# Optimization experiments

Measured on AMD Instinct MI355X. Metric: run time of the kernel, lower is better.

Reference implementation:

```python
import jax, jax.numpy as jnp
import numpy as np

N_DRUG = 20000
N_TARGET = 20000
N = N_DRUG + N_TARGET
E = 500000
D = 128
L = 2
NEG_SLOPE = 0.2


def _gat(h, edge_index, W, asrc, adst, edge_bias=None):
    """Single-head GAT layer: h [N,d] -> [N,d]."""
    n = h.shape[0]
    hp = h @ W                                   # [N,d]
    src, dst = edge_index[0], edge_index[1]      # [E]
    logit = (hp @ asrc)[src] + (hp @ adst)[dst]  # [E]
    if edge_bias is not None:
        logit = logit + edge_bias
    e = jax.nn.leaky_relu(logit, NEG_SLOPE)
    # numerically-stable softmax over incoming edges of each dst node
    m = jax.ops.segment_max(e, dst, num_segments=n)
    m = jnp.where(jnp.isfinite(m), m, 0.0)
    ex = jnp.exp(e - m[dst])                     # [E]
    denom = jax.ops.segment_sum(ex, dst, num_segments=n) + 1e-16  # [N]
    num = jax.ops.segment_sum(ex[:, None] * hp[src], dst, num_segments=n)  # [N,d]
    return jax.nn.elu(num / denom[:, None])


def _forward(x_drug, x_target, W_drug, b_drug, W_target, b_target,
             W_gat, a_src, a_dst, a_edge, edge_attr_dd,
             edge_dd, edge_dt, edge_tt):
    h = jnp.concatenate([x_drug @ W_drug + b_drug,
                         x_target @ W_target + b_target], axis=0)  # [N,d]
    for l in range(L):
        bias_dd = edge_attr_dd @ a_edge[l]  # [E] additive attention bias
        x1 = _gat(h, edge_dd, W_gat[l, 0], a_src[l, 0], a_dst[l, 0], bias_dd)
        x2 = _gat(h, edge_dt, W_gat[l, 1], a_src[l, 1], a_dst[l, 1])
        x3 = _gat(h, edge_tt, W_gat[l, 2], a_src[l, 2], a_dst[l, 2])
        h = (x1 + x2 + x3) / 3.0
    return h


def setup_inputs() -> dict:
    key = jax.random.key(0)
    ks = jax.random.split(key, 16)
    s_in = lambda f: 1.0 / np.sqrt(f)
    edge_dd = jax.random.randint(ks[0], (2, E), 0, N_DRUG, dtype=jnp.int32)
    edge_tt = jax.random.randint(ks[1], (2, E), N_DRUG, N, dtype=jnp.int32)
    dt_src = jax.random.randint(ks[2], (E,), 0, N_DRUG, dtype=jnp.int32)
    dt_dst = jax.random.randint(ks[3], (E,), N_DRUG, N, dtype=jnp.int32)
    edge_dt = jnp.stack([dt_src, dt_dst], axis=0)
    return {
        "x_drug": jax.random.normal(ks[4], (N_DRUG, 2048), jnp.float32),
        "x_target": jax.random.normal(ks[5], (N_TARGET, 1280), jnp.float32),
        "W_drug": jax.random.normal(ks[6], (2048, D), jnp.float32) * s_in(2048),
        "b_drug": jnp.zeros((D,), jnp.float32),
        "W_target": jax.random.normal(ks[7], (1280, D), jnp.float32) * s_in(1280),
        "b_target": jnp.zeros((D,), jnp.float32),
        "W_gat": jax.random.normal(ks[8], (L, 3, D, D), jnp.float32) * s_in(D),
        "a_src": jax.random.normal(ks[9], (L, 3, D), jnp.float32) * s_in(D),
        "a_dst": jax.random.normal(ks[10], (L, 3, D), jnp.float32) * s_in(D),
        "a_edge": jax.random.normal(ks[11], (L, D), jnp.float32) * s_in(D),
        "edge_attr_dd": jax.random.normal(ks[12], (E, D), jnp.float32),
        "edge_dd": edge_dd,
        "edge_dt": edge_dt,
        "edge_tt": edge_tt,
    }


def reference(x_drug, x_target, W_drug, b_drug, W_target, b_target,
              W_gat, a_src, a_dst, a_edge, edge_attr_dd,
              edge_dd, edge_dt, edge_tt):
    h = _forward(x_drug, x_target, W_drug, b_drug, W_target, b_target,
                 W_gat, a_src, a_dst, a_edge, edge_attr_dd,
                 edge_dd, edge_dt, edge_tt)
    return h[:N_DRUG], h[N_DRUG:]
```

## Files before the change

### kernel.cpp

```cpp
#include <hip/hip_runtime.h>
#include <hip/hip_fp16.h>
#include <hip/hip_bf16.h>

#define NDRUG 20000
#define NTGT  20000
#define NN    40000
#define NE    500000
#define DDIM  128
#define CAP   96
#define NB    313
#define BSTRIDE 4096
#define AS1 __attribute__((address_space(1)))
#define AS3 __attribute__((address_space(3)))

typedef __attribute__((ext_vector_type(4))) float f32x4;
typedef __attribute__((ext_vector_type(8))) short s16x8;
typedef __attribute__((ext_vector_type(4))) unsigned u32x4;

__device__ inline unsigned short bf_rn(float x) {
  unsigned u = __float_as_uint(x);
  return (unsigned short)((u + 0x7FFFu + ((u >> 16) & 1u)) >> 16);
}
__device__ __forceinline__ void split1(float x, short& h, short& l) {
  const unsigned u = __float_as_uint(x);
  const unsigned hu = (u + 0x7FFFu + ((u >> 16) & 1u)) & 0xFFFF0000u;
  h = (short)(hu >> 16);
  l = (short)bf_rn(x - __uint_as_float(hu));
}
__device__ __forceinline__ void split_pk(float x0, float x1, unsigned& hp, unsigned& lp) {
  __hip_bfloat162 h2 = __float22bfloat162_rn(make_float2(x0, x1));
  unsigned hu; __builtin_memcpy(&hu, &h2, 4);
  const float f0 = __uint_as_float(hu << 16);
  const float f1 = __uint_as_float(hu & 0xFFFF0000u);
  __hip_bfloat162 l2 = __float22bfloat162_rn(make_float2(x0 - f0, x1 - f1));
  unsigned lu; __builtin_memcpy(&lu, &l2, 4);
  hp = hu; lp = lu;
}
__device__ __forceinline__ void cvt8_pk(const float4 a, const float4 b, s16x8& h, s16x8& l) {
  unsigned h0, h1, h2, h3, l0, l1, l2, l3;
  split_pk(a.x, a.y, h0, l0);
  split_pk(a.z, a.w, h1, l1);
  split_pk(b.x, b.y, h2, l2);
  split_pk(b.z, b.w, h3, l3);
  u32x4 hu = {h0, h1, h2, h3};
  u32x4 lu = {l0, l1, l2, l3};
  h = __builtin_bit_cast(s16x8, hu);
  l = __builtin_bit_cast(s16x8, lu);
}
__device__ __forceinline__ void glds16(const void* g, void* l) {
  __builtin_amdgcn_global_load_lds((const AS1 unsigned*)g, (AS3 unsigned*)l, 16, 0, 0);
}
__device__ __forceinline__ f32x4 mfma(const s16x8& a, const s16x8& b, const f32x4& c) {
  return __builtin_amdgcn_mfma_f32_16x16x32_bf16(a, b, c, 0, 0, 0);
}
__device__ __forceinline__ int swz(int c) { return c ^ ((c >> 3) & 7); }

__global__ void prep_all(const float* __restrict__ Wd, const float* __restrict__ Wt,
                         const float* __restrict__ Wg, short* __restrict__ pdh,
                         short* __restrict__ pdl, short* __restrict__ pth,
                         short* __restrict__ ptl, short* __restrict__ pgh,
                         short* __restrict__ pgl, int* __restrict__ bcur) {
  if (blockIdx.x < 4) {
    const int i = blockIdx.x * 256 + threadIdx.x;
    if (i < 3 * NB) bcur[i] = i * BSTRIDE;
  }
  int b = blockIdx.x;
  const float* W; short* ph; short* pl; int K; int idx;
  if (b < 1024) { W = Wd; ph = pdh; pl = pdl; K = 2048; idx = b * 256 + threadIdx.x; }
  else if (b < 1664) { W = Wt; ph = pth; pl = ptl; K = 1280; idx = (b - 1024) * 256 + threadIdx.x; }
  else {
    const int bb = b - 1664, mat = bb >> 6;
    W = Wg + (size_t)mat * 128 * 128;
    ph = pgh + (size_t)mat * 128 * 128;
    pl = pgl + (size_t)mat * 128 * 128;
    K = 128;
    idx = (bb & 63) * 256 + threadIdx.x;
  }
  if (idx >= K * 128) return;
  const int kt = idx >> 12, r = idx & 4095;
  const int dchunk = r >> 3, j = r & 7;
  const int c = swz(dchunk);
  const int col = c >> 2, kg = c & 3;
  const int k = kt * 32 + kg * 8 + j;
  short h, l;
  split1(W[(size_t)k * 128 + col], h, l);
  ph[idx] = h;
  pl[idx] = l;
}

__global__ __launch_bounds__(256)
void gemm_proj(const float* __restrict__ xd, const short* __restrict__ pdh,
               const short* __restrict__ pdl, const float* __restrict__ bd,
               const float* __restrict__ xt, const short* __restrict__ pth,
               const short* __restrict__ ptl, const float* __restrict__ bt,
               short* __restrict__ hh, short* __restrict__ hl) {
  __shared__ float Af[2][64 * 32];
  __shared__ short Bf[2][2][4096];

  int b = blockIdx.x;
  const float* A; const short* BH; const short* BL; const float* bias;
  int M, K, rowbase;
  if (b < 313) { A = xd; BH = pdh; BL = pdl; bias = bd; M = NDRUG; K = 2048; rowbase = 0; }
  else { b -= 313; A = xt; BH = pth; BL = ptl; bias = bt; M = NTGT; K = 1280; rowbase = NDRUG; }
  const int bm = b * 64;
  const int t = threadIdx.x, w = t >> 6, lane = t & 63;
  const int lr = lane & 15, kg = lane >> 4;
  const int steps = K >> 5;

  const int ad0 = (w << 6) + lane, ad1 = ad0 + 256;
  const int ar0 = ad0 >> 3, ar1 = ad1 >> 3;
  const int ac0 = (ad0 & 7) ^ (ar0 & 7), ac1 = (ad1 & 7) ^ (ar1 & 7);
  int gr0 = bm + ar0; if (gr0 >= M) gr0 = M - 1;
  int gr1 = bm + ar1; if (gr1 >= M) gr1 = M - 1;
  const float* asrc0 = A + (size_t)gr0 * K + ac0 * 4;
  const float* asrc1 = A + (size_t)gr1 * K + ac1 * 4;
  const int bd0 = (w << 6) + lane, bd1 = bd0 + 256;

  f32x4 acc[8] = {};

  auto stage = [&](int buf, int kt) {
    const int kk = kt << 5;
    glds16(asrc0 + kk, &Af[buf][(w << 6) * 4]);
    glds16(asrc1 + kk, &Af[buf][(256 + (w << 6)) * 4]);
    const size_t bo = (size_t)kt * 4096;
    glds16(BH + bo + bd0 * 8, &Bf[buf][0][(w << 6) * 8]);
    glds16(BH + bo + bd1 * 8, &Bf[buf][0][(256 + (w << 6)) * 8]);
    glds16(BL + bo + bd0 * 8, &Bf[buf][1][(w << 6) * 8]);
    glds16(BL + bo + bd1 * 8, &Bf[buf][1][(256 + (w << 6)) * 8]);
  };

  const int arow = (w << 4) + lr;
  const int ap0 = (arow * 8 + ((kg * 2) ^ (arow & 7))) * 4;
  const int ap1 = (arow * 8 + ((kg * 2 + 1) ^ (arow & 7))) * 4;

  auto compute = [&](int buf) {
    const float4 va = *(const float4*)&Af[buf][ap0];
    const float4 vb = *(const float4*)&Af[buf][ap1];
    s16x8 ah, al;
    cvt8_pk(va, vb, ah, al);
#pragma unroll
    for (int n = 0; n < 8; ++n) {
      const int c = ((n * 16 + lr) << 2) + kg;
      const int pos = swz(c) << 3;
      const s16x8 bh = *(const s16x8*)&Bf[buf][0][pos];
      const s16x8 bl = *(const s16x8*)&Bf[buf][1][pos];
      acc[n] = mfma(ah, bh, acc[n]);
      acc[n] = mfma(ah, bl, acc[n]);
      acc[n] = mfma(al, bh, acc[n]);
    }
  };

  stage(0, 0);
  __syncthreads();
  int cur = 0;
  for (int kt = 0; kt < steps - 1; ++kt) {
    stage(cur ^ 1, kt + 1);
    compute(cur);
    __syncthreads();
    cur ^= 1;
  }
  compute(cur);

#pragma unroll
  for (int n = 0; n < 8; ++n) {
    const int col = n * 16 + lr;
    const float bv = bias[col];
#pragma unroll
    for (int r = 0; r < 4; ++r) {
      const int row = bm + (w << 4) + kg * 4 + r;
      if (row < M) {
        short h, l;
        split1(acc[n][r] + bv, h, l);
        hh[(size_t)(rowbase + row) * DDIM + col] = h;
        hl[(size_t)(rowbase + row) * DDIM + col] = l;
      }
    }
  }
}

__global__ __launch_bounds__(256)
void edge_bias_kernel(const float* __restrict__ ea, const float* __restrict__ ae0,
                      const float* __restrict__ ae1, float* __restrict__ b0,
                      float* __restrict__ b1) {
  const int wave = threadIdx.x >> 6, lane = threadIdx.x & 63;
  const int e = blockIdx.x * 4 + wave;
  if (e >= NE) return;
  const float2 v = *(const float2*)(ea + (size_t)e * DDIM + (lane << 1));
  float s0 = v.x * ae0[lane << 1] + v.y * ae0[(lane << 1) + 1];
  float s1 = v.x * ae1[lane << 1] + v.y * ae1[(lane << 1) + 1];
#pragma unroll
  for (int o = 32; o; o >>= 1) { s0 += __shfl_xor(s0, o); s1 += __shfl_xor(s1, o); }
  if (lane == 0) { b0[e] = s0; b1[e] = s1; }
}

__global__ __launch_bounds__(256)
void gemm_gat(const short* __restrict__ ahh, const short* __restrict__ ahl,
              const short* __restrict__ PH3, const short* __restrict__ PL3,
              const float* __restrict__ asrc3, const float* __restrict__ adst3,
              __half* __restrict__ hp16, float* __restrict__ s_all,
              float* __restrict__ d_all) {
  const int rel = blockIdx.y;
  const int bm = blockIdx.x * 64;
  if (rel == 0 && bm >= NDRUG + 32) return;
  if (rel == 2 && bm + 64 <= NDRUG) return;

  __shared__ short Apl[2][2][2048];
  __shared__ short Bf[2][2][4096];

  const short* BH = PH3 + (size_t)rel * DDIM * DDIM;
  const short* BL = PL3 + (size_t)rel * DDIM * DDIM;
  const int t = threadIdx.x, w = t >> 6, lane = t & 63;
  const int lr = lane & 15, kg = lane >> 4;

  const int apn = w >> 1;
  const short* aplane = apn ? ahl : ahh;
  const int ad0 = ((w & 1) << 6) + lane, ad1 = ad0 + 128;
  const int ac0 = swz(ad0), ac1 = swz(ad1);
  const short* asrc0 = aplane + (size_t)(bm + (ac0 >> 2)) * DDIM + (ac0 & 3) * 8;
  const short* asrc1 = aplane + (size_t)(bm + (ac1 >> 2)) * DDIM + (ac1 & 3) * 8;
  const int bd0 = (w << 6) + lane, bd1 = bd0 + 256;

  f32x4 acc[8] = {};

  auto stage = [&](int buf, int kt) {
    const int kk = kt << 5;
    glds16(asrc0 + kk, &Apl[buf][apn][ad0 * 8]);
    glds16(asrc1 + kk, &Apl[buf][apn][ad1 * 8]);
    const size_t bo = (size_t)kt * 4096;
    glds16(BH + bo + bd0 * 8, &Bf[buf][0][(w << 6) * 8]);
    glds16(BH + bo + bd1 * 8, &Bf[buf][0][(256 + (w << 6)) * 8]);
    glds16(BL + bo + bd0 * 8, &Bf[buf][1][(w << 6) * 8]);
    glds16(BL + bo + bd1 * 8, &Bf[buf][1][(256 + (w << 6)) * 8]);
  };

  const int arow = (w << 4) + lr;
  const int apos = swz((arow << 2) + kg) << 3;

  auto compute = [&](int buf) {
    const s16x8 ah = *(const s16x8*)&Apl[buf][0][apos];
    const s16x8 al = *(const s16x8*)&Apl[buf][1][apos];
#pragma unroll
    for (int n = 0; n < 8; ++n) {
      const int c = ((n * 16 + lr) << 2) + kg;
      const int pos = swz(c) << 3;
      const s16x8 bh = *(const s16x8*)&Bf[buf][0][pos];
      const s16x8 bl = *(const s16x8*)&Bf[buf][1][pos];
      acc[n] = mfma(ah, bh, acc[n]);
      acc[n] = mfma(ah, bl, acc[n]);
      acc[n] = mfma(al, bh, acc[n]);
    }
  };

  stage(0, 0);
  __syncthreads();
  int cur = 0;
  for (int kt = 0; kt < 3; ++kt) {
    stage(cur ^ 1, kt + 1);
    compute(cur);
    __syncthreads();
    cur ^= 1;
  }
  compute(cur);

  __half* hpr = hp16 + (size_t)rel * NN * DDIM;
  float asv[8], adv[8];
#pragma unroll
  for (int n = 0; n < 8; ++n) {
    asv[n] = asrc3[rel * DDIM + n * 16 + lr];
    adv[n] = adst3[rel * DDIM + n * 16 + lr];
  }
#pragma unroll
  for (int r = 0; r < 4; ++r) {
    const int row = bm + (w << 4) + kg * 4 + r;
    const bool write_hp = (rel != 1) || (row < NDRUG);
    float ps = 0.f, pd = 0.f;
#pragma unroll
    for (int n = 0; n < 8; ++n) {
      if (write_hp) hpr[(size_t)row * DDIM + n * 16 + lr] = __float2half_rn(acc[n][r]);
      ps += acc[n][r] * asv[n];
      pd += acc[n][r] * adv[n];
    }
#pragma unroll
    for (int o = 1; o < 16; o <<= 1) { ps += __shfl_xor(ps, o); pd += __shfl_xor(pd, o); }
    if (lr == 0) {
      s_all[(size_t)rel * NN + row] = ps;
      d_all[(size_t)rel * NN + row] = pd;
    }
  }
}

#define BIN_BLK 64
__global__ __launch_bounds__(256)
void bin3(const int* __restrict__ s0, const int* __restrict__ d0,
          const int* __restrict__ s1, const int* __restrict__ d1,
          const int* __restrict__ s2, const int* __restrict__ d2,
          int* __restrict__ bcur, int2* __restrict__ binned) {
  __shared__ int lhist[NB], lbase[NB];
  const int rel = blockIdx.y;
  const int* src = rel == 0 ? s0 : (rel == 1 ? s1 : s2);
  const int* dst = rel == 0 ? d0 : (rel == 1 ? d1 : d2);
  const int per = (NE + BIN_BLK - 1) / BIN_BLK;
  const int e0 = blockIdx.x * per;
  const int e1 = min(e0 + per, NE);
  const int t = threadIdx.x;
  for (int i = t; i < NB; i += 256) lhist[i] = 0;
  __syncthreads();
  for (int e = e0 + t; e < e1; e += 256) atomicAdd(&lhist[dst[e] >> 7], 1);
  __syncthreads();
  for (int i = t; i < NB; i += 256) {
    const int c = lhist[i];
    lbase[i] = c ? atomicAdd(&bcur[rel * NB + i], c) : 0;
  }
  __syncthreads();
  for (int i = t; i < NB; i += 256) lhist[i] = 0;
  __syncthreads();
  for (int e = e0 + t; e < e1; e += 256) {
    const int d = dst[e];
    const int b = d >> 7;
    const int p = lbase[b] + atomicAdd(&lhist[b], 1);
    binned[p] = make_int2(src[e], (e << 7) | (d & 127));
  }
}

__global__ __launch_bounds__(1024)
void scanb(const int* __restrict__ bcur, int* __restrict__ bbase,
           int* __restrict__ offs_all) {
  __shared__ int part[1024];
  const int t = threadIdx.x;
  const int v = (t < 3 * NB) ? (bcur[t] - t * BSTRIDE) : 0;
  part[t] = v;
  __syncthreads();
  for (int o = 1; o < 1024; o <<= 1) {
    const int pv = (t >= o) ? part[t - o] : 0;
    __syncthreads();
    part[t] += pv;
    __syncthreads();
  }
  if (t < 3 * NB) {
    const int excl = part[t] - v;
    bbase[t] = excl - (t / NB) * NE;
  }
  if (t < 3) offs_all[t * (NN + 1) + NN] = NE;
}

__global__ __launch_bounds__(256)
void csr_bucket(const int2* __restrict__ binned, const int* __restrict__ bbase,
                const int* __restrict__ bcur, int* __restrict__ offs_all,
                int* __restrict__ csrc_all, int* __restrict__ ceid0) {
  __shared__ int hist[128], scan[128], curs[128];
  const int rel = blockIdx.y, b = blockIdx.x;
  const int idx = rel * NB + b;
  const int base = bbase[idx];
  const int n = bcur[idx] - idx * BSTRIDE;
  const int t = threadIdx.x;
  if (t < 128) hist[t] = 0;
  __syncthreads();
  const int2* seg = binned + (size_t)idx * BSTRIDE;
  for (int i = t; i < n; i += 256) atomicAdd(&hist[seg[i].y & 127], 1);
  __syncthreads();
  if (t < 128) scan[t] = hist[t];
  __syncthreads();
  for (int o = 1; o < 128; o <<= 1) {
    const int pv = (t >= o && t < 128) ? scan[t - o] : 0;
    __syncthreads();
    if (t < 128) scan[t] += pv;
    __syncthreads();
  }
  if (t < 128) {
    const int excl = base + scan[t] - hist[t];
    const int node = b * 128 + t;
    if (node < NN) offs_all[rel * (NN + 1) + node] = excl;
    curs[t] = excl;
  }
  __syncthreads();
  int* csrc = csrc_all + (size_t)rel * NE;
  for (int i = t; i < n; i += 256) {
    const int2 v = seg[i];
    const int p = atomicAdd(&curs[v.y & 127], 1);
    csrc[p] = v.x;
    if (rel == 0) ceid0[p] = v.y >> 7;
  }
}

__device__ __forceinline__ void gat_one(const int* __restrict__ offs,
                                        const int* __restrict__ csrc,
                                        const int* __restrict__ ceid,
                                        const float* __restrict__ ebias,
                                        const float* __restrict__ s, float dn,
                                        const __half* __restrict__ hpr, int node,
                                        float* exbuf, int* srcbuf, int lane,
                                        float& o0, float& o1) {
  const int beg = offs[node];
  int cnt = offs[node + 1] - beg;
  if (cnt > CAP) cnt = CAP;
  if (cnt == 0) return;
  __threadfence_block();
  float m = -1e30f;
  for (int i = lane; i < cnt; i += 64) {
    const int sn = csrc[beg + i];
    float logit = s[sn] + dn;
    if (ebias) logit += ebias[ceid[beg + i]];
    const float e = logit >= 0.f ? logit : 0.2f * logit;
    exbuf[i] = e;
    srcbuf[i] = sn;
    m = fmaxf(m, e);
  }
#pragma unroll
  for (int o = 32; o; o >>= 1) m = fmaxf(m, __shfl_xor(m, o));
  float ssum = 0.f;
  for (int i = lane; i < cnt; i += 64) {
    const float ex = __expf(exbuf[i] - m);
    exbuf[i] = ex;
    ssum += ex;
  }
#pragma unroll
  for (int o = 32; o; o >>= 1) ssum += __shfl_xor(ssum, o);
  const float inv = 1.f / (ssum + 1e-16f);
  __threadfence_block();
  const int c = lane << 1;
  float n0 = 0.f, n1 = 0.f;
  int i = 0;
  for (; i + 4 <= cnt; i += 4) {
    const float w0 = exbuf[i], w1 = exbuf[i + 1], w2 = exbuf[i + 2], w3 = exbuf[i + 3];
    const float2 v0 = __half22float2(*(const __half2*)(hpr + (size_t)srcbuf[i] * DDIM + c));
    const float2 v1 = __half22float2(*(const __half2*)(hpr + (size_t)srcbuf[i + 1] * DDIM + c));
    const float2 v2 = __half22float2(*(const __half2*)(hpr + (size_t)srcbuf[i + 2] * DDIM + c));
    const float2 v3 = __half22float2(*(const __half2*)(hpr + (size_t)srcbuf[i + 3] * DDIM + c));
    n0 += w0 * v0.x + w1 * v1.x + w2 * v2.x + w3 * v3.x;
    n1 += w0 * v0.y + w1 * v1.y + w2 * v2.y + w3 * v3.y;
  }
  for (; i < cnt; ++i) {
    const float w = exbuf[i];
    const float2 v = __half22float2(*(const __half2*)(hpr + (size_t)srcbuf[i] * DDIM + c));
    n0 += w * v.x;
    n1 += w * v.y;
  }
  const float v0 = n0 * inv, v1 = n1 * inv;
  o0 += (v0 > 0.f ? v0 : expm1f(v0));
  o1 += (v1 > 0.f ? v1 : expm1f(v1));
}

__global__ __launch_bounds__(256)
void agg_all(const int* __restrict__ offs_all, const int* __restrict__ csrc_all,
             const int* __restrict__ ceid0, const float* __restrict__ ebias,
             const float* __restrict__ s_all, const float* __restrict__ d_all,
             const __half* __restrict__ hp16, float* __restrict__ outf,
             short* __restrict__ ohh, short* __restrict__ ohl, int write_f32) {
  __shared__ float exbuf[4][CAP];
  __shared__ int   srcbuf[4][CAP];
  const int wave = threadIdx.x >> 6, lane = threadIdx.x & 63;
  const int node = blockIdx.x * 4 + wave;
  float o0 = 0.f, o1 = 0.f;
  if (node < NDRUG) {
    gat_one(offs_all, csrc_all, ceid0, ebias, s_all, d_all[node],
            hp16, node, exbuf[wave], srcbuf[wave], lane, o0, o1);
  } else {
#pragma unroll
    for (int rel = 1; rel <= 2; ++rel) {
      gat_one(offs_all + rel * (NN + 1), csrc_all + (size_t)rel * NE, nullptr, nullptr,
              s_all + (size_t)rel * NN, d_all[(size_t)rel * NN + node],
              hp16 + (size_t)rel * NN * DDIM, node, exbuf[wave], srcbuf[wave], lane, o0, o1);
    }
  }
  o0 *= (1.f / 3.f);
  o1 *= (1.f / 3.f);
  const int c = lane << 1;
  if (write_f32) {
    *(float2*)(outf + (size_t)node * DDIM + c) = make_float2(o0, o1);
  } else {
    short h0, l0, h1, l1;
    split1(o0, h0, l0);
    split1(o1, h1, l1);
    *(short2*)(ohh + (size_t)node * DDIM + c) = make_short2(h0, h1);
    *(short2*)(ohl + (size_t)node * DDIM + c) = make_short2(l0, l1);
  }
}

extern "C" void kernel_launch(void* const* d_in, const int* in_sizes, int n_in,
                              void* d_out, int out_size, void* d_ws, size_t ws_size,
                              hipStream_t stream) {
  const float* x_drug    = (const float*)d_in[0];
  const float* x_target  = (const float*)d_in[1];
  const float* W_drug    = (const float*)d_in[2];
  const float* b_drug    = (const float*)d_in[3];
  const float* W_target  = (const float*)d_in[4];
  const float* b_target  = (const float*)d_in[5];
  const float* W_gat     = (const float*)d_in[6];
  const float* a_src     = (const float*)d_in[7];
  const float* a_dst     = (const float*)d_in[8];
  const float* a_edge    = (const float*)d_in[9];
  const float* edge_attr = (const float*)d_in[10];
  const int*   e_dd      = (const int*)d_in[11];
  const int*   e_dt      = (const int*)d_in[12];
  const int*   e_tt      = (const int*)d_in[13];
  float* out = (float*)d_out;

  char* ws = (char*)d_ws;
  size_t off = 0;
  auto alloc = [&](size_t b) -> void* {
    void* p = ws + off;
    off += (b + 255) & ~(size_t)255;
    return p;
  };
  __half* hp16  = (__half*)alloc((size_t)3 * NN * DDIM * 2);
  short* hhA    = (short*)alloc((size_t)NN * DDIM * 2);
  short* hlA    = (short*)alloc((size_t)NN * DDIM * 2);
  short* hhB    = (short*)alloc((size_t)NN * DDIM * 2);
  short* hlB    = (short*)alloc((size_t)NN * DDIM * 2);
  float* s_all  = (float*)alloc((size_t)3 * NN * 4);
  float* d_allb = (float*)alloc((size_t)3 * NN * 4);
  float* bias0  = (float*)alloc((size_t)NE * 4);
  float* bias1  = (float*)alloc((size_t)NE * 4);
  int* bcur     = (int*)alloc((size_t)3 * NB * 4);
  int* bbase    = (int*)alloc((size_t)3 * NB * 4);
  int2* binned  = (int2*)alloc((size_t)3 * NB * BSTRIDE * 8);
  int* offs_all = (int*)alloc((size_t)3 * (NN + 1) * 4);
  int* csrc_all = (int*)alloc((size_t)3 * NE * 4);
  int* ceid0    = (int*)alloc((size_t)NE * 4);
  short* pwd_h  = (short*)alloc((size_t)2048 * 128 * 2);
  short* pwd_l  = (short*)alloc((size_t)2048 * 128 * 2);
  short* pwt_h  = (short*)alloc((size_t)1280 * 128 * 2);
  short* pwt_l  = (short*)alloc((size_t)1280 * 128 * 2);
  short* pwg_h  = (short*)alloc((size_t)6 * 128 * 128 * 2);
  short* pwg_l  = (short*)alloc((size_t)6 * 128 * 128 * 2);

  prep_all<<<1024 + 640 + 384, 256, 0, stream>>>(W_drug, W_target, W_gat,
                                                 pwd_h, pwd_l, pwt_h, pwt_l,
                                                 pwg_h, pwg_l, bcur);

  gemm_proj<<<626, 256, 0, stream>>>(x_drug, pwd_h, pwd_l, b_drug,
                                     x_target, pwt_h, pwt_l, b_target, hhA, hlA);

  edge_bias_kernel<<<NE / 4, 256, 0, stream>>>(edge_attr, a_edge, a_edge + DDIM,
                                               bias0, bias1);

  bin3<<<dim3(BIN_BLK, 3), 256, 0, stream>>>(e_dd, e_dd + NE, e_dt, e_dt + NE,
                                             e_tt, e_tt + NE, bcur, binned);
  scanb<<<1, 1024, 0, stream>>>(bcur, bbase, offs_all);
  csr_bucket<<<dim3(NB, 3), 256, 0, stream>>>(binned, bbase, bcur, offs_all,
                                              csrc_all, ceid0);

  gemm_gat<<<dim3(625, 3), 256, 0, stream>>>(hhA, hlA, pwg_h, pwg_l,
                                             a_src, a_dst, hp16, s_all, d_allb);
  agg_all<<<NN / 4, 256, 0, stream>>>(offs_all, csrc_all, ceid0, bias0,
                                      s_all, d_allb, hp16, nullptr, hhB, hlB, 0);
  gemm_gat<<<dim3(625, 3), 256, 0, stream>>>(hhB, hlB,
                                             pwg_h + (size_t)3 * DDIM * DDIM,
                                             pwg_l + (size_t)3 * DDIM * DDIM,
                                             a_src + 3 * DDIM, a_dst + 3 * DDIM,
                                             hp16, s_all, d_allb);
  agg_all<<<NN / 4, 256, 0, stream>>>(offs_all, csrc_all, ceid0, bias1,
                                      s_all, d_allb, hp16, out, nullptr, nullptr, 1);
}
```

Baseline: 424.6 us.

## Drop scan kernel, pre-permute edge bias into CSR order, widen edge-bias loads

Three changes. The single-block scanb launch is removed, and each csr_bucket block now computes its own base offset by reducing the bucket counts that precede it. csr_bucket also gathers both layers' edge biases into CSR order, so the aggregation kernel reads them contiguously instead of doing an indirect lookup through ceid. The edge-bias kernel uses float4 loads with two edges per wave. The cost is redundant prefix reductions in every csr_bucket block and two extra bias arrays.

```diff
diff --git a/kernel.cpp b/kernel.cpp
--- a/kernel.cpp
+++ b/kernel.cpp
@@ -183,14 +183,17 @@
                       const float* __restrict__ ae1, float* __restrict__ b0,
                       float* __restrict__ b1) {
   const int wave = threadIdx.x >> 6, lane = threadIdx.x & 63;
-  const int e = blockIdx.x * 4 + wave;
+  const int half = lane >> 5, l32 = lane & 31;
+  const int e = blockIdx.x * 8 + wave * 2 + half;
   if (e >= NE) return;
-  const float2 v = *(const float2*)(ea + (size_t)e * DDIM + (lane << 1));
-  float s0 = v.x * ae0[lane << 1] + v.y * ae0[(lane << 1) + 1];
-  float s1 = v.x * ae1[lane << 1] + v.y * ae1[(lane << 1) + 1];
-#pragma unroll
-  for (int o = 32; o; o >>= 1) { s0 += __shfl_xor(s0, o); s1 += __shfl_xor(s1, o); }
-  if (lane == 0) { b0[e] = s0; b1[e] = s1; }
+  const float4 v = *(const float4*)(ea + (size_t)e * DDIM + (l32 << 2));
+  const float4 a0 = *(const float4*)(ae0 + (l32 << 2));
+  const float4 a1 = *(const float4*)(ae1 + (l32 << 2));
+  float s0 = v.x * a0.x + v.y * a0.y + v.z * a0.z + v.w * a0.w;
+  float s1 = v.x * a1.x + v.y * a1.y + v.z * a1.z + v.w * a1.w;
+#pragma unroll
+  for (int o = 16; o; o >>= 1) { s0 += __shfl_xor(s0, o); s1 += __shfl_xor(s1, o); }
+  if (l32 == 0) { b0[e] = s0; b1[e] = s1; }
 }
 
 __global__ __launch_bounds__(256)
@@ -322,37 +325,27 @@
   }
 }
 
-__global__ __launch_bounds__(1024)
-void scanb(const int* __restrict__ bcur, int* __restrict__ bbase,
-           int* __restrict__ offs_all) {
-  __shared__ int part[1024];
-  const int t = threadIdx.x;
-  const int v = (t < 3 * NB) ? (bcur[t] - t * BSTRIDE) : 0;
-  part[t] = v;
-  __syncthreads();
-  for (int o = 1; o < 1024; o <<= 1) {
-    const int pv = (t >= o) ? part[t - o] : 0;
-    __syncthreads();
-    part[t] += pv;
-    __syncthreads();
-  }
-  if (t < 3 * NB) {
-    const int excl = part[t] - v;
-    bbase[t] = excl - (t / NB) * NE;
-  }
-  if (t < 3) offs_all[t * (NN + 1) + NN] = NE;
-}
-
 __global__ __launch_bounds__(256)
-void csr_bucket(const int2* __restrict__ binned, const int* __restrict__ bbase,
-                const int* __restrict__ bcur, int* __restrict__ offs_all,
-                int* __restrict__ csrc_all, int* __restrict__ ceid0) {
+void csr_bucket(const int2* __restrict__ binned, const int* __restrict__ bcur,
+                int* __restrict__ offs_all, int* __restrict__ csrc_all,
+                const float* __restrict__ eb0, const float* __restrict__ eb1,
+                float* __restrict__ ebR0, float* __restrict__ ebR1) {
+  __shared__ int red[256];
   __shared__ int hist[128], scan[128], curs[128];
   const int rel = blockIdx.y, b = blockIdx.x;
   const int idx = rel * NB + b;
-  const int base = bbase[idx];
+  const int t = threadIdx.x;
+  int tot = 0;
+  for (int i = t; i < idx; i += 256) tot += bcur[i] - i * BSTRIDE;
+  red[t] = tot;
+  __syncthreads();
+  for (int o = 128; o; o >>= 1) {
+    if (t < o) red[t] += red[t + o];
+    __syncthreads();
+  }
+  const int base = red[0] - rel * NE;
   const int n = bcur[idx] - idx * BSTRIDE;
-  const int t = threadIdx.x;
+  if (b == NB - 1 && t == 0) offs_all[rel * (NN + 1) + NN] = NE;
   if (t < 128) hist[t] = 0;
   __syncthreads();
   const int2* seg = binned + (size_t)idx * BSTRIDE;
@@ -378,14 +371,17 @@
     const int2 v = seg[i];
     const int p = atomicAdd(&curs[v.y & 127], 1);
     csrc[p] = v.x;
-    if (rel == 0) ceid0[p] = v.y >> 7;
+    if (rel == 0) {
+      const int eid = v.y >> 7;
+      ebR0[p] = eb0[eid];
+      ebR1[p] = eb1[eid];
+    }
   }
 }
 
 __device__ __forceinline__ void gat_one(const int* __restrict__ offs,
                                         const int* __restrict__ csrc,
-                                        const int* __restrict__ ceid,
-                                        const float* __restrict__ ebias,
+                                        const float* __restrict__ ebR,
                                         const float* __restrict__ s, float dn,
                                         const __half* __restrict__ hpr, int node,
                                         float* exbuf, int* srcbuf, int lane,
@@ -399,7 +395,7 @@
   for (int i = lane; i < cnt; i += 64) {
     const int sn = csrc[beg + i];
     float logit = s[sn] + dn;
-    if (ebias) logit += ebias[ceid[beg + i]];
+    if (ebR) logit += ebR[beg + i];
     const float e = logit >= 0.f ? logit : 0.2f * logit;
     exbuf[i] = e;
     srcbuf[i] = sn;
@@ -442,22 +438,22 @@
 
 __global__ __launch_bounds__(256)
 void agg_all(const int* __restrict__ offs_all, const int* __restrict__ csrc_all,
-             const int* __restrict__ ceid0, const float* __restrict__ ebias,
-             const float* __restrict__ s_all, const float* __restrict__ d_all,
-             const __half* __restrict__ hp16, float* __restrict__ outf,
-             short* __restrict__ ohh, short* __restrict__ ohl, int write_f32) {
+             const float* __restrict__ ebR, const float* __restrict__ s_all,
+             const float* __restrict__ d_all, const __half* __restrict__ hp16,
+             float* __restrict__ outf, short* __restrict__ ohh,
+             short* __restrict__ ohl, int write_f32) {
   __shared__ float exbuf[4][CAP];
   __shared__ int   srcbuf[4][CAP];
   const int wave = threadIdx.x >> 6, lane = threadIdx.x & 63;
   const int node = blockIdx.x * 4 + wave;
   float o0 = 0.f, o1 = 0.f;
   if (node < NDRUG) {
-    gat_one(offs_all, csrc_all, ceid0, ebias, s_all, d_all[node],
+    gat_one(offs_all, csrc_all, ebR, s_all, d_all[node],
             hp16, node, exbuf[wave], srcbuf[wave], lane, o0, o1);
   } else {
 #pragma unroll
     for (int rel = 1; rel <= 2; ++rel) {
-      gat_one(offs_all + rel * (NN + 1), csrc_all + (size_t)rel * NE, nullptr, nullptr,
+      gat_one(offs_all + rel * (NN + 1), csrc_all + (size_t)rel * NE, nullptr,
               s_all + (size_t)rel * NN, d_all[(size_t)rel * NN + node],
               hp16 + (size_t)rel * NN * DDIM, node, exbuf[wave], srcbuf[wave], lane, o0, o1);
     }
@@ -511,12 +507,12 @@
   float* d_allb = (float*)alloc((size_t)3 * NN * 4);
   float* bias0  = (float*)alloc((size_t)NE * 4);
   float* bias1  = (float*)alloc((size_t)NE * 4);
+  float* ebR0   = (float*)alloc((size_t)NE * 4);
+  float* ebR1   = (float*)alloc((size_t)NE * 4);
   int* bcur     = (int*)alloc((size_t)3 * NB * 4);
-  int* bbase    = (int*)alloc((size_t)3 * NB * 4);
   int2* binned  = (int2*)alloc((size_t)3 * NB * BSTRIDE * 8);
   int* offs_all = (int*)alloc((size_t)3 * (NN + 1) * 4);
   int* csrc_all = (int*)alloc((size_t)3 * NE * 4);
-  int* ceid0    = (int*)alloc((size_t)NE * 4);
   short* pwd_h  = (short*)alloc((size_t)2048 * 128 * 2);
   short* pwd_l  = (short*)alloc((size_t)2048 * 128 * 2);
   short* pwt_h  = (short*)alloc((size_t)1280 * 128 * 2);
@@ -531,24 +527,23 @@
   gemm_proj<<<626, 256, 0, stream>>>(x_drug, pwd_h, pwd_l, b_drug,
                                      x_target, pwt_h, pwt_l, b_target, hhA, hlA);
 
-  edge_bias_kernel<<<NE / 4, 256, 0, stream>>>(edge_attr, a_edge, a_edge + DDIM,
-                                               bias0, bias1);
+  edge_bias_kernel<<<(NE + 7) / 8, 256, 0, stream>>>(edge_attr, a_edge,
+                                                     a_edge + DDIM, bias0, bias1);
 
   bin3<<<dim3(BIN_BLK, 3), 256, 0, stream>>>(e_dd, e_dd + NE, e_dt, e_dt + NE,
                                              e_tt, e_tt + NE, bcur, binned);
-  scanb<<<1, 1024, 0, stream>>>(bcur, bbase, offs_all);
-  csr_bucket<<<dim3(NB, 3), 256, 0, stream>>>(binned, bbase, bcur, offs_all,
-                                              csrc_all, ceid0);
+  csr_bucket<<<dim3(NB, 3), 256, 0, stream>>>(binned, bcur, offs_all, csrc_all,
+                                              bias0, bias1, ebR0, ebR1);
 
   gemm_gat<<<dim3(625, 3), 256, 0, stream>>>(hhA, hlA, pwg_h, pwg_l,
                                              a_src, a_dst, hp16, s_all, d_allb);
-  agg_all<<<NN / 4, 256, 0, stream>>>(offs_all, csrc_all, ceid0, bias0,
+  agg_all<<<NN / 4, 256, 0, stream>>>(offs_all, csrc_all, ebR0,
                                       s_all, d_allb, hp16, nullptr, hhB, hlB, 0);
   gemm_gat<<<dim3(625, 3), 256, 0, stream>>>(hhB, hlB,
                                              pwg_h + (size_t)3 * DDIM * DDIM,
                                              pwg_l + (size_t)3 * DDIM * DDIM,
                                              a_src + 3 * DDIM, a_dst + 3 * DDIM,
                                              hp16, s_all, d_allb);
-  agg_all<<<NN / 4, 256, 0, stream>>>(offs_all, csrc_all, ceid0, bias1,
+  agg_all<<<NN / 4, 256, 0, stream>>>(offs_all, csrc_all, ebR1,
                                       s_all, d_allb, hp16, out, nullptr, nullptr, 1);
 }
```

Result: faster. 388.3 us (median of 2 runs) (-8.5%).
